# Performance work log

Measured on AMD Instinct MI355X. Metric: run time of the kernel, lower is better.

Reference implementation:

```python
import jax, jax.numpy as jnp
import numpy as np

SEQ_LEN = 256
INPUT_DIM = 1
HIDDEN = 2048
CLASSES = 10
BATCH = 128


def setup_inputs() -> dict:
    key = jax.random.key(0)
    ks = jax.random.split(key, 6)
    x = jax.random.normal(ks[0], (BATCH, SEQ_LEN), dtype=jnp.float32)
    # Gate order along the 4H axis: g (cell candidate), i, f, o.
    Wx = jax.random.normal(ks[1], (INPUT_DIM, 4 * HIDDEN), dtype=jnp.float32) * 0.1
    Wh = jax.random.normal(ks[2], (HIDDEN, 4 * HIDDEN), dtype=jnp.float32) * (1.0 / np.sqrt(HIDDEN))
    b = jax.random.normal(ks[3], (4 * HIDDEN,), dtype=jnp.float32) * 0.1
    Wph = jax.random.normal(ks[4], (HIDDEN, CLASSES), dtype=jnp.float32) * (1.0 / np.sqrt(HIDDEN))
    bp = jax.random.normal(ks[5], (CLASSES,), dtype=jnp.float32) * 0.1
    return {"x": x, "Wx": Wx, "Wh": Wh, "b": b, "Wph": Wph, "bp": bp}


def reference(x, Wx, Wh, b, Wph, bp):
    B, T = x.shape
    H = Wh.shape[0]
    # Original loops over seq_length - 1 timesteps.
    xs = x[:, : T - 1].T[:, :, None]  # [T-1, B, 1]

    def step(carry, x_t):
        h, c = carry
        z = x_t @ Wx + h @ Wh + b  # [B, 4H] fused gate GEMM
        g = jnp.tanh(z[:, 0 * H:1 * H])
        i = jax.nn.sigmoid(z[:, 1 * H:2 * H])
        f = jax.nn.sigmoid(z[:, 2 * H:3 * H])
        o = jax.nn.sigmoid(z[:, 3 * H:4 * H])
        c = g * i + c * f
        h = jnp.tanh(c) * o
        return (h, c), None

    h0 = jnp.zeros((B, H), dtype=x.dtype)
    c0 = jnp.zeros((B, H), dtype=x.dtype)
    (h, _), _ = jax.lax.scan(step, (h0, c0), xs)
    logits = h @ Wph + bp
    return jax.nn.softmax(logits, axis=1)
```

## Files before the change

kernel.cpp:

```cpp
#include <hip/hip_runtime.h>
#include <hip/hip_bf16.h>

#define SEQ_LEN 256
#define HIDDEN  2048
#define CLASSES 10
#define BATCH   128
#define NWG     256
#define WG_THREADS 512
#define STEPS   (SEQ_LEN - 1)
#define KTILES  64
#define PF      16
#define LDS_WH  131072
#define LDS_ALL (LDS_WH + 4096)

typedef __attribute__((ext_vector_type(8))) short  bf16x8;
typedef __attribute__((ext_vector_type(8))) unsigned short u16x8;
typedef __attribute__((ext_vector_type(4))) float  f32x4;
typedef __attribute__((ext_vector_type(4))) unsigned int u32x4;

#define WHP_OFF  0
#define HB_OFF   33554432UL
#define HF_OFF   (HB_OFF + 4UL * 524288UL)
#define BAR_OFF  (HF_OFF + 1048576UL)

__device__ __forceinline__ unsigned short f2bf(float f) {
    unsigned int u = __float_as_uint(f);
    return (unsigned short)((u + 0x7FFFu + ((u >> 16) & 1u)) >> 16);
}
__device__ __forceinline__ float sigm(float z)  { return 1.0f / (1.0f + __expf(-z)); }
__device__ __forceinline__ float tanh_f(float z){ return 2.0f / (1.0f + __expf(-2.0f * z)) - 1.0f; }

__device__ __forceinline__ unsigned int aload(const unsigned int* p) {
    return __hip_atomic_load(p, __ATOMIC_RELAXED, __HIP_MEMORY_SCOPE_AGENT);
}
__device__ __forceinline__ void astore(unsigned int* p, unsigned int v) {
    __hip_atomic_store(p, v, __ATOMIC_RELAXED, __HIP_MEMORY_SCOPE_AGENT);
}

__global__ void lstm_pack_kernel(const float* __restrict__ Wh,
                                 unsigned short* __restrict__ whp,
                                 unsigned short* __restrict__ hbufs,
                                 unsigned int* __restrict__ bar) {
    int chunk = blockIdx.x * 256 + threadIdx.x;
    int lane = chunk & 63;
    int nt   = (chunk >> 6) & 1;
    int kt   = (chunk >> 7) & 63;
    int W    = chunk >> 13;
    int q = lane >> 4, l16 = lane & 15;
    int c32  = nt * 16 + l16;
    int gate = c32 >> 3, u = c32 & 7;
    int n    = gate * 2048 + W * 8 + u;
    int k0   = kt * 32 + q * 8;
    u16x8 frag;
    #pragma unroll
    for (int j = 0; j < 8; ++j)
        frag[j] = f2bf(Wh[(size_t)(k0 + j) * 8192 + n]);
    ((u16x8*)whp)[chunk] = frag;

    if (chunk < 32768) ((u32x4*)hbufs)[chunk] = (u32x4){0, 0, 0, 0};
    if (chunk < 2048) bar[chunk] = 0u;
}

__device__ __forceinline__ void grid_barrier(unsigned int* bar, unsigned int phase,
                                             bool do_inv, int W) {
    __syncthreads();
    if (threadIdx.x < 64) {
        const int lane = threadIdx.x;
        if (lane == 0) astore(&bar[W], phase);
        if (W < 8) {
            unsigned int* sl = &bar[W * 32 + (lane & 31)];
            while (!__all((int)(aload(sl) >= phase)))
                __builtin_amdgcn_s_sleep(1);
            if (lane == 0) astore(&bar[512 + 16 * W], phase);
            if (W == 0) {
                unsigned int* dn = &bar[512 + 16 * (lane & 7)];
                while (!__all((int)(aload(dn) >= phase)))
                    __builtin_amdgcn_s_sleep(1);
                if (lane < 32) astore(&bar[1024 + 16 * lane], phase);
            }
        }
        if (lane == 0 && W != 0) {
            unsigned int* rl = &bar[1024 + 16 * (W & 31)];
            while (aload(rl) < phase)
                __builtin_amdgcn_s_sleep(1);
        }
        if (do_inv)
            __builtin_amdgcn_fence(__ATOMIC_ACQUIRE, "agent");
    }
    __syncthreads();
}

__global__ __launch_bounds__(WG_THREADS, 2) void lstm_persist(
    const float* __restrict__ x,  const float* __restrict__ Wx,
    const float* __restrict__ b,  const float* __restrict__ Wph,
    const float* __restrict__ bp, const unsigned short* __restrict__ whp,
    unsigned short* hbufs, float* hfin,
    unsigned int* bar, float* out)
{
    extern __shared__ char lds[];
    const int tid = threadIdx.x;
    const int W   = blockIdx.x;

    {
        const u32x4* src = (const u32x4*)whp + (size_t)W * 8192;
        u32x4* dst = (u32x4*)lds;
        for (int i = tid; i < 8192; i += WG_THREADS) dst[i] = src[i];
    }
    unsigned short* hstage = (unsigned short*)(lds + LDS_WH);
    __syncthreads();

    const int lane = tid & 63;
    const int wv   = tid >> 6;
    const int q    = lane >> 4;
    const int l16  = lane & 15;
    const int s    = (lane >> 3) & 1;
    const int u    = lane & 7;
    const int rowA = wv * 16 + l16;
    const int row0 = wv * 16 + q * 4;
    const int colh = W * 8 + u;

    const int n0 = ((l16) >> 3) * 2048 + W * 8 + (l16 & 7);
    const int n1 = ((16 + l16) >> 3) * 2048 + W * 8 + ((16 + l16) & 7);
    const float wx0 = Wx[n0], bb0 = b[n0];
    const float wx1 = Wx[n1], bb1 = b[n1];

    const int abase = q * 128 + rowA;

    float c_state[4] = {0.f, 0.f, 0.f, 0.f};

    for (int t = 0; t < STEPS; ++t) {
        unsigned short* hcur  = hbufs + (size_t)(t & 3) * 262144;
        unsigned short* hnext = hbufs + (size_t)((t + 1) & 3) * 262144;

        const bf16x8* hc8 = (const bf16x8*)hcur;
        const char* lp = lds + lane * 16;

        float xv[4];
        #pragma unroll
        for (int r = 0; r < 4; ++r) xv[r] = x[(row0 + r) * SEQ_LEN + t];

        bf16x8 a_pf[PF];
        #pragma unroll
        for (int i = 0; i < PF; ++i)
            a_pf[i] = hc8[abase + i * 512];

        f32x4 acc0 = {0.f, 0.f, 0.f, 0.f};
        f32x4 acc1 = {0.f, 0.f, 0.f, 0.f};
        #pragma unroll 16
        for (int kt = 0; kt < KTILES; ++kt) {
            bf16x8 a_cur = a_pf[kt & (PF - 1)];
            int nk = kt + PF;
            if (nk > KTILES - 1) nk = KTILES - 1;
            a_pf[kt & (PF - 1)] = hc8[abase + nk * 512];
            bf16x8 b0 = *(const bf16x8*)(lp + (kt * 2 + 0) * 1024);
            bf16x8 b1 = *(const bf16x8*)(lp + (kt * 2 + 1) * 1024);
            acc0 = __builtin_amdgcn_mfma_f32_16x16x32_bf16(a_cur, b0, acc0, 0, 0, 0);
            acc1 = __builtin_amdgcn_mfma_f32_16x16x32_bf16(a_cur, b1, acc1, 0, 0, 0);
        }

        const bool last = (t == STEPS - 1);
        #pragma unroll
        for (int r = 0; r < 4; ++r) {
            float z0 = acc0[r] + xv[r] * wx0 + bb0;
            float z1 = acc1[r] + xv[r] * wx1 + bb1;
            float p0 = __shfl_xor(z0, 8, 64);
            float p1 = __shfl_xor(z1, 8, 64);
            float zg = s ? p0 : z0;
            float zi = s ? z0 : p0;
            float zf = s ? p1 : z1;
            float zo = s ? z1 : p1;
            float cn = tanh_f(zg) * sigm(zi) + c_state[r] * sigm(zf);
            c_state[r] = cn;
            float h = tanh_f(cn) * sigm(zo);
            if (s == 0) {
                hstage[(row0 + r) * 8 + u] = f2bf(h);
                if (last)
                    __hip_atomic_store(&hfin[(row0 + r) * HIDDEN + colh], h,
                                       __ATOMIC_RELAXED, __HIP_MEMORY_SCOPE_AGENT);
            }
        }
        __syncthreads();
        astore(&((unsigned int*)hnext)[W * 512 + tid],
               ((const unsigned int*)hstage)[tid]);
        grid_barrier(bar, (unsigned int)(t + 1), (t & 3) == 2 || last, W);
    }

    if (W < BATCH) {
        float part[CLASSES];
        #pragma unroll
        for (int c = 0; c < CLASSES; ++c) part[c] = 0.f;
        for (int k = tid; k < HIDDEN; k += WG_THREADS) {
            float hv = hfin[W * HIDDEN + k];
            #pragma unroll
            for (int c = 0; c < CLASSES; ++c) part[c] += hv * Wph[k * CLASSES + c];
        }
        #pragma unroll
        for (int c = 0; c < CLASSES; ++c)
            for (int off = 32; off > 0; off >>= 1)
                part[c] += __shfl_xor(part[c], off, 64);
        float* red = (float*)(lds + LDS_WH);
        __syncthreads();
        if (lane == 0)
            for (int c = 0; c < CLASSES; ++c) red[wv * CLASSES + c] = part[c];
        __syncthreads();
        if (tid == 0) {
            float lg[CLASSES];
            for (int c = 0; c < CLASSES; ++c) {
                float sm = bp[c];
                for (int w8 = 0; w8 < 8; ++w8) sm += red[w8 * CLASSES + c];
                lg[c] = sm;
            }
            float mx = lg[0];
            for (int c = 1; c < CLASSES; ++c) mx = fmaxf(mx, lg[c]);
            float se = 0.f;
            for (int c = 0; c < CLASSES; ++c) { lg[c] = __expf(lg[c] - mx); se += lg[c]; }
            float inv = 1.0f / se;
            for (int c = 0; c < CLASSES; ++c) out[W * CLASSES + c] = lg[c] * inv;
        }
    }
}

extern "C" void kernel_launch(void* const* d_in, const int* in_sizes, int n_in,
                              void* d_out, int out_size, void* d_ws, size_t ws_size,
                              hipStream_t stream) {
    const float* x   = (const float*)d_in[0];
    const float* Wx  = (const float*)d_in[1];
    const float* Wh  = (const float*)d_in[2];
    const float* b   = (const float*)d_in[3];
    const float* Wph = (const float*)d_in[4];
    const float* bp  = (const float*)d_in[5];
    float* out = (float*)d_out;

    char* ws = (char*)d_ws;
    unsigned short* whp  = (unsigned short*)(ws + WHP_OFF);
    unsigned short* hbufs= (unsigned short*)(ws + HB_OFF);
    float*          hfin = (float*)(ws + HF_OFF);
    unsigned int*   bar  = (unsigned int*)(ws + BAR_OFF);

    hipFuncSetAttribute((const void*)lstm_persist,
                        hipFuncAttributeMaxDynamicSharedMemorySize, LDS_ALL);

    lstm_pack_kernel<<<8192, 256, 0, stream>>>(Wh, whp, hbufs, bar);
    lstm_persist<<<NWG, WG_THREADS, LDS_ALL, stream>>>(x, Wx, b, Wph, bp,
                                                       whp, hbufs, hfin, bar, out);
}
```

Before: 2.471 ms.

## Flatten grid barrier to direct all-slot polling and split MFMA accumulator chains

Replaces the two-level tree grid barrier, where leader workgroups gather arrivals and broadcast a release flag, with a flat scheme. Every workgroup's first wavefront polls all 256 arrival slots directly, four per lane. The intent is to remove the serial gather-then-release hops on the per-timestep critical path, at the cost of many more atomic loads hitting the same cache lines. It also splits each MFMA accumulator into two interleaved chains so that dependent MFMAs can overlap, then sums them at the end.

```diff
diff --git a/kernel.cpp b/kernel.cpp
--- a/kernel.cpp
+++ b/kernel.cpp
@@ -67,22 +67,15 @@
     if (threadIdx.x < 64) {
         const int lane = threadIdx.x;
         if (lane == 0) astore(&bar[W], phase);
-        if (W < 8) {
-            unsigned int* sl = &bar[W * 32 + (lane & 31)];
-            while (!__all((int)(aload(sl) >= phase)))
-                __builtin_amdgcn_s_sleep(1);
-            if (lane == 0) astore(&bar[512 + 16 * W], phase);
-            if (W == 0) {
-                unsigned int* dn = &bar[512 + 16 * (lane & 7)];
-                while (!__all((int)(aload(dn) >= phase)))
-                    __builtin_amdgcn_s_sleep(1);
-                if (lane < 32) astore(&bar[1024 + 16 * lane], phase);
-            }
-        }
-        if (lane == 0 && W != 0) {
-            unsigned int* rl = &bar[1024 + 16 * (W & 31)];
-            while (aload(rl) < phase)
-                __builtin_amdgcn_s_sleep(1);
+        const unsigned int* sl = &bar[lane * 4];
+        for (;;) {
+            unsigned int a0 = aload(sl + 0);
+            unsigned int a1 = aload(sl + 1);
+            unsigned int a2 = aload(sl + 2);
+            unsigned int a3 = aload(sl + 3);
+            bool ok = (a0 >= phase) & (a1 >= phase) & (a2 >= phase) & (a3 >= phase);
+            if (__all((int)ok)) break;
+            __builtin_amdgcn_s_sleep(1);
         }
         if (do_inv)
             __builtin_amdgcn_fence(__ATOMIC_ACQUIRE, "agent");
@@ -144,8 +137,10 @@
         for (int i = 0; i < PF; ++i)
             a_pf[i] = hc8[abase + i * 512];
 
-        f32x4 acc0 = {0.f, 0.f, 0.f, 0.f};
-        f32x4 acc1 = {0.f, 0.f, 0.f, 0.f};
+        f32x4 acc0a = {0.f, 0.f, 0.f, 0.f};
+        f32x4 acc0b = {0.f, 0.f, 0.f, 0.f};
+        f32x4 acc1a = {0.f, 0.f, 0.f, 0.f};
+        f32x4 acc1b = {0.f, 0.f, 0.f, 0.f};
         #pragma unroll 16
         for (int kt = 0; kt < KTILES; ++kt) {
             bf16x8 a_cur = a_pf[kt & (PF - 1)];
@@ -154,9 +149,16 @@
             a_pf[kt & (PF - 1)] = hc8[abase + nk * 512];
             bf16x8 b0 = *(const bf16x8*)(lp + (kt * 2 + 0) * 1024);
             bf16x8 b1 = *(const bf16x8*)(lp + (kt * 2 + 1) * 1024);
-            acc0 = __builtin_amdgcn_mfma_f32_16x16x32_bf16(a_cur, b0, acc0, 0, 0, 0);
-            acc1 = __builtin_amdgcn_mfma_f32_16x16x32_bf16(a_cur, b1, acc1, 0, 0, 0);
-        }
+            if (kt & 1) {
+                acc0b = __builtin_amdgcn_mfma_f32_16x16x32_bf16(a_cur, b0, acc0b, 0, 0, 0);
+                acc1b = __builtin_amdgcn_mfma_f32_16x16x32_bf16(a_cur, b1, acc1b, 0, 0, 0);
+            } else {
+                acc0a = __builtin_amdgcn_mfma_f32_16x16x32_bf16(a_cur, b0, acc0a, 0, 0, 0);
+                acc1a = __builtin_amdgcn_mfma_f32_16x16x32_bf16(a_cur, b1, acc1a, 0, 0, 0);
+            }
+        }
+        f32x4 acc0 = acc0a + acc0b;
+        f32x4 acc1 = acc1a + acc1b;
 
         const bool last = (t == STEPS - 1);
         #pragma unroll
```

After: 3.242 ms. 1.31x slower.

## Split K dimension across paired workgroups with partial-sum exchange

Applied to the files above, without the earlier changes.

Each workgroup now computes half of the K reduction (1024 of 2048) for the columns of two owners: its own and those of its partner W^8. Weights are repacked so each workgroup holds both owners' columns for its K half. The partial sums for the partner's columns go out through global memory, followed by a pairwise flag handshake before the gate math. This halves the per-workgroup serial K loop and the h loads, at the cost of an extra pairwise sync and a global partial-sum round trip every step.

```diff
diff --git a/kernel.cpp b/kernel.cpp
--- a/kernel.cpp
+++ b/kernel.cpp
@@ -8,8 +8,8 @@
 #define NWG     256
 #define WG_THREADS 512
 #define STEPS   (SEQ_LEN - 1)
-#define KTILES  64
-#define PF      16
+#define KTILES_H 32
+#define PF      8
 #define LDS_WH  131072
 #define LDS_ALL (LDS_WH + 4096)
 
@@ -22,6 +22,7 @@
 #define HB_OFF   33554432UL
 #define HF_OFF   (HB_OFF + 4UL * 524288UL)
 #define BAR_OFF  (HF_OFF + 1048576UL)
+#define PART_OFF (BAR_OFF + 65536UL)
 
 __device__ __forceinline__ unsigned short f2bf(float f) {
     unsigned int u = __float_as_uint(f);
@@ -34,6 +35,12 @@
     return __hip_atomic_load(p, __ATOMIC_RELAXED, __HIP_MEMORY_SCOPE_AGENT);
 }
 __device__ __forceinline__ void astore(unsigned int* p, unsigned int v) {
+    __hip_atomic_store(p, v, __ATOMIC_RELAXED, __HIP_MEMORY_SCOPE_AGENT);
+}
+__device__ __forceinline__ float aloadf(const float* p) {
+    return __hip_atomic_load(p, __ATOMIC_RELAXED, __HIP_MEMORY_SCOPE_AGENT);
+}
+__device__ __forceinline__ void astoref(float* p, float v) {
     __hip_atomic_store(p, v, __ATOMIC_RELAXED, __HIP_MEMORY_SCOPE_AGENT);
 }
 
@@ -43,14 +50,16 @@
                                  unsigned int* __restrict__ bar) {
     int chunk = blockIdx.x * 256 + threadIdx.x;
     int lane = chunk & 63;
-    int nt   = (chunk >> 6) & 1;
-    int kt   = (chunk >> 7) & 63;
+    int s    = (chunk >> 6) & 127;
     int W    = chunk >> 13;
+    int kt = s >> 2, nt = s & 3;
+    int kh = (W >> 3) & 1;
+    int owner = (W & ~8) | ((nt & 2) << 2);
     int q = lane >> 4, l16 = lane & 15;
-    int c32  = nt * 16 + l16;
-    int gate = c32 >> 3, u = c32 & 7;
-    int n    = gate * 2048 + W * 8 + u;
-    int k0   = kt * 32 + q * 8;
+    int gate = (nt & 1) * 2 + (l16 >> 3);
+    int u = l16 & 7;
+    int n = gate * 2048 + owner * 8 + u;
+    int k0 = kh * 1024 + kt * 32 + q * 8;
     u16x8 frag;
     #pragma unroll
     for (int j = 0; j < 8; ++j)
@@ -58,7 +67,7 @@
     ((u16x8*)whp)[chunk] = frag;
 
     if (chunk < 32768) ((u32x4*)hbufs)[chunk] = (u32x4){0, 0, 0, 0};
-    if (chunk < 2048) bar[chunk] = 0u;
+    if (chunk < 8192) bar[chunk] = 0u;
 }
 
 __device__ __forceinline__ void grid_barrier(unsigned int* bar, unsigned int phase,
@@ -95,7 +104,7 @@
     const float* __restrict__ b,  const float* __restrict__ Wph,
     const float* __restrict__ bp, const unsigned short* __restrict__ whp,
     unsigned short* hbufs, float* hfin,
-    unsigned int* bar, float* out)
+    unsigned int* bar, float* part, float* out)
 {
     extern __shared__ char lds[];
     const int tid = threadIdx.x;
@@ -119,12 +128,17 @@
     const int row0 = wv * 16 + q * 4;
     const int colh = W * 8 + u;
 
+    const int sel  = (W >> 3) & 1;
+    const int koff = sel * 32;
+    float* psend = part + ((size_t)(W ^ 8) * 512 + tid) * 8;
+    float* precv = part + ((size_t)W * 512 + tid) * 8;
+
     const int n0 = ((l16) >> 3) * 2048 + W * 8 + (l16 & 7);
     const int n1 = ((16 + l16) >> 3) * 2048 + W * 8 + ((16 + l16) & 7);
     const float wx0 = Wx[n0], bb0 = b[n0];
     const float wx1 = Wx[n1], bb1 = b[n1];
 
-    const int abase = q * 128 + rowA;
+    const int abase = koff * 512 + q * 128 + rowA;
 
     float c_state[4] = {0.f, 0.f, 0.f, 0.f};
 
@@ -146,23 +160,53 @@
 
         f32x4 acc0 = {0.f, 0.f, 0.f, 0.f};
         f32x4 acc1 = {0.f, 0.f, 0.f, 0.f};
-        #pragma unroll 16
-        for (int kt = 0; kt < KTILES; ++kt) {
+        f32x4 acc2 = {0.f, 0.f, 0.f, 0.f};
+        f32x4 acc3 = {0.f, 0.f, 0.f, 0.f};
+        #pragma unroll 8
+        for (int kt = 0; kt < KTILES_H; ++kt) {
             bf16x8 a_cur = a_pf[kt & (PF - 1)];
             int nk = kt + PF;
-            if (nk > KTILES - 1) nk = KTILES - 1;
+            if (nk > KTILES_H - 1) nk = KTILES_H - 1;
             a_pf[kt & (PF - 1)] = hc8[abase + nk * 512];
-            bf16x8 b0 = *(const bf16x8*)(lp + (kt * 2 + 0) * 1024);
-            bf16x8 b1 = *(const bf16x8*)(lp + (kt * 2 + 1) * 1024);
+            bf16x8 b0 = *(const bf16x8*)(lp + (kt * 4 + 0) * 1024);
+            bf16x8 b1 = *(const bf16x8*)(lp + (kt * 4 + 1) * 1024);
+            bf16x8 b2 = *(const bf16x8*)(lp + (kt * 4 + 2) * 1024);
+            bf16x8 b3 = *(const bf16x8*)(lp + (kt * 4 + 3) * 1024);
             acc0 = __builtin_amdgcn_mfma_f32_16x16x32_bf16(a_cur, b0, acc0, 0, 0, 0);
             acc1 = __builtin_amdgcn_mfma_f32_16x16x32_bf16(a_cur, b1, acc1, 0, 0, 0);
+            acc2 = __builtin_amdgcn_mfma_f32_16x16x32_bf16(a_cur, b2, acc2, 0, 0, 0);
+            acc3 = __builtin_amdgcn_mfma_f32_16x16x32_bf16(a_cur, b3, acc3, 0, 0, 0);
+        }
+
+        {
+            f32x4 s0 = sel ? acc0 : acc2;
+            f32x4 s1 = sel ? acc1 : acc3;
+            #pragma unroll
+            for (int j = 0; j < 4; ++j) {
+                astoref(&psend[j],     s0[j]);
+                astoref(&psend[4 + j], s1[j]);
+            }
+        }
+        __syncthreads();
+        if (tid == 0) {
+            astore(&bar[2048 + 16 * W], (unsigned int)(t + 1));
+            while (aload(&bar[2048 + 16 * (W ^ 8)]) < (unsigned int)(t + 1))
+                __builtin_amdgcn_s_sleep(1);
+        }
+        __syncthreads();
+        f32x4 m0 = sel ? acc2 : acc0;
+        f32x4 m1 = sel ? acc3 : acc1;
+        #pragma unroll
+        for (int j = 0; j < 4; ++j) {
+            m0[j] += aloadf(&precv[j]);
+            m1[j] += aloadf(&precv[4 + j]);
         }
 
         const bool last = (t == STEPS - 1);
         #pragma unroll
         for (int r = 0; r < 4; ++r) {
-            float z0 = acc0[r] + xv[r] * wx0 + bb0;
-            float z1 = acc1[r] + xv[r] * wx1 + bb1;
+            float z0 = m0[r] + xv[r] * wx0 + bb0;
+            float z1 = m1[r] + xv[r] * wx1 + bb1;
             float p0 = __shfl_xor(z0, 8, 64);
             float p1 = __shfl_xor(z1, 8, 64);
             float zg = s ? p0 : z0;
@@ -186,22 +230,22 @@
     }
 
     if (W < BATCH) {
-        float part[CLASSES];
-        #pragma unroll
-        for (int c = 0; c < CLASSES; ++c) part[c] = 0.f;
+        float part_[CLASSES];
+        #pragma unroll
+        for (int c = 0; c < CLASSES; ++c) part_[c] = 0.f;
         for (int k = tid; k < HIDDEN; k += WG_THREADS) {
             float hv = hfin[W * HIDDEN + k];
             #pragma unroll
-            for (int c = 0; c < CLASSES; ++c) part[c] += hv * Wph[k * CLASSES + c];
+            for (int c = 0; c < CLASSES; ++c) part_[c] += hv * Wph[k * CLASSES + c];
         }
         #pragma unroll
         for (int c = 0; c < CLASSES; ++c)
             for (int off = 32; off > 0; off >>= 1)
-                part[c] += __shfl_xor(part[c], off, 64);
+                part_[c] += __shfl_xor(part_[c], off, 64);
         float* red = (float*)(lds + LDS_WH);
         __syncthreads();
         if (lane == 0)
-            for (int c = 0; c < CLASSES; ++c) red[wv * CLASSES + c] = part[c];
+            for (int c = 0; c < CLASSES; ++c) red[wv * CLASSES + c] = part_[c];
         __syncthreads();
         if (tid == 0) {
             float lg[CLASSES];
@@ -236,11 +280,12 @@
     unsigned short* hbufs= (unsigned short*)(ws + HB_OFF);
     float*          hfin = (float*)(ws + HF_OFF);
     unsigned int*   bar  = (unsigned int*)(ws + BAR_OFF);
+    float*          part = (float*)(ws + PART_OFF);
 
     hipFuncSetAttribute((const void*)lstm_persist,
                         hipFuncAttributeMaxDynamicSharedMemorySize, LDS_ALL);
 
     lstm_pack_kernel<<<8192, 256, 0, stream>>>(Wh, whp, hbufs, bar);
     lstm_persist<<<NWG, WG_THREADS, LDS_ALL, stream>>>(x, Wx, b, Wph, bp,
-                                                       whp, hbufs, hfin, bar, out);
-}
+                                                       whp, hbufs, hfin, bar, part, out);
+}
```

After: 4.149 ms. +67.9%, slower.

## Replace per-step grid barrier with per-workgroup dataflow flags and staggered K order

Applied to the files above, without the earlier changes.

Removes the global grid barrier from each timestep. Each workgroup now publishes a per-WG step flag after writing its slice of h, and consumers poll only the flags for the K-tiles they are about to read. The K loop start is rotated per workgroup (kt0 = W>>2), so workgroups begin on different tiles and can start on data that is already ready, overlapping compute with straggling producers. The cost is extra flag polling inside the MFMA loop and a periodic acquire fence every 4 steps. This relies on memory-ordering assumptions across the 4-deep h ring buffer, which is a correctness risk.

```diff
diff --git a/kernel.cpp b/kernel.cpp
--- a/kernel.cpp
+++ b/kernel.cpp
@@ -12,6 +12,7 @@
 #define PF      16
 #define LDS_WH  131072
 #define LDS_ALL (LDS_WH + 4096)
+#define FLAGS   2048
 
 typedef __attribute__((ext_vector_type(8))) short  bf16x8;
 typedef __attribute__((ext_vector_type(8))) unsigned short u16x8;
@@ -58,7 +59,7 @@
     ((u16x8*)whp)[chunk] = frag;
 
     if (chunk < 32768) ((u32x4*)hbufs)[chunk] = (u32x4){0, 0, 0, 0};
-    if (chunk < 2048) bar[chunk] = 0u;
+    if (chunk < 8192) bar[chunk] = 0u;
 }
 
 __device__ __forceinline__ void grid_barrier(unsigned int* bar, unsigned int phase,
@@ -118,6 +119,7 @@
     const int rowA = wv * 16 + l16;
     const int row0 = wv * 16 + q * 4;
     const int colh = W * 8 + u;
+    const int kt0  = W >> 2;
 
     const int n0 = ((l16) >> 3) * 2048 + W * 8 + (l16 & 7);
     const int n1 = ((16 + l16) >> 3) * 2048 + W * 8 + ((16 + l16) & 7);
@@ -126,9 +128,18 @@
 
     const int abase = q * 128 + rowA;
 
+    const int fsub = (lane & 15) >> 2;
+    const int fj   = lane & 3;
+
     float c_state[4] = {0.f, 0.f, 0.f, 0.f};
 
     for (int t = 0; t < STEPS; ++t) {
+        if ((t & 3) == 0) {
+            if (tid < 64)
+                __builtin_amdgcn_fence(__ATOMIC_ACQUIRE, "agent");
+            __syncthreads();
+        }
+
         unsigned short* hcur  = hbufs + (size_t)(t & 3) * 262144;
         unsigned short* hnext = hbufs + (size_t)((t + 1) & 3) * 262144;
 
@@ -139,21 +150,46 @@
         #pragma unroll
         for (int r = 0; r < 4; ++r) xv[r] = x[(row0 + r) * SEQ_LEN + t];
 
+        {
+            const int kti = (kt0 + (lane >> 2)) & 63;
+            const unsigned int* fp = &bar[FLAGS + 16 * (4 * kti + fj)];
+            while (!__all((int)(aload(fp) >= (unsigned int)t)))
+                __builtin_amdgcn_s_sleep(2);
+            __asm__ __volatile__("" ::: "memory");
+        }
+        unsigned int fcur;
+        {
+            const int kti = (kt0 + PF + fsub) & 63;
+            fcur = aload(&bar[FLAGS + 16 * (4 * kti + fj)]);
+        }
+
         bf16x8 a_pf[PF];
         #pragma unroll
         for (int i = 0; i < PF; ++i)
-            a_pf[i] = hc8[abase + i * 512];
+            a_pf[i] = hc8[abase + ((kt0 + i) & 63) * 512];
 
         f32x4 acc0 = {0.f, 0.f, 0.f, 0.f};
         f32x4 acc1 = {0.f, 0.f, 0.f, 0.f};
         #pragma unroll 16
         for (int kt = 0; kt < KTILES; ++kt) {
+            if ((kt & 3) == 0 && kt < KTILES - PF) {
+                if (!__all((int)(fcur >= (unsigned int)t))) {
+                    const int kti = (kt0 + kt + PF + fsub) & 63;
+                    const unsigned int* fp = &bar[FLAGS + 16 * (4 * kti + fj)];
+                    while (!__all((int)(aload(fp) >= (unsigned int)t)))
+                        __builtin_amdgcn_s_sleep(2);
+                }
+                __asm__ __volatile__("" ::: "memory");
+                const int kti = (kt0 + kt + PF + 4 + fsub) & 63;
+                fcur = aload(&bar[FLAGS + 16 * (4 * kti + fj)]);
+            }
+            const int k63 = (kt0 + kt) & 63;
             bf16x8 a_cur = a_pf[kt & (PF - 1)];
             int nk = kt + PF;
             if (nk > KTILES - 1) nk = KTILES - 1;
-            a_pf[kt & (PF - 1)] = hc8[abase + nk * 512];
-            bf16x8 b0 = *(const bf16x8*)(lp + (kt * 2 + 0) * 1024);
-            bf16x8 b1 = *(const bf16x8*)(lp + (kt * 2 + 1) * 1024);
+            a_pf[kt & (PF - 1)] = hc8[abase + ((kt0 + nk) & 63) * 512];
+            bf16x8 b0 = *(const bf16x8*)(lp + (k63 * 2 + 0) * 1024);
+            bf16x8 b1 = *(const bf16x8*)(lp + (k63 * 2 + 1) * 1024);
             acc0 = __builtin_amdgcn_mfma_f32_16x16x32_bf16(a_cur, b0, acc0, 0, 0, 0);
             acc1 = __builtin_amdgcn_mfma_f32_16x16x32_bf16(a_cur, b1, acc1, 0, 0, 0);
         }
@@ -182,8 +218,12 @@
         __syncthreads();
         astore(&((unsigned int*)hnext)[W * 512 + tid],
                ((const unsigned int*)hstage)[tid]);
-        grid_barrier(bar, (unsigned int)(t + 1), (t & 3) == 2 || last, W);
-    }
+        __syncthreads();
+        if (tid == 0)
+            astore(&bar[FLAGS + 16 * W], (unsigned int)(t + 1));
+    }
+
+    grid_barrier(bar, 1u, true, W);
 
     if (W < BATCH) {
         float part[CLASSES];
```

After: 2.829 ms. 14.5% more time.
